# Kernel tuning notes

Hardware: AMD Instinct MI355X
Metric: run time of the kernel (lower is better)

Reference implementation:

```python
import jax, jax.numpy as jnp
import numpy as np

N, IN, HID, OUT, C, H = 50000, 1488, 1024, 512, 32, 8
E = 800000

def setup_inputs() -> dict:
    key = jax.random.key(0)
    ks = jax.random.split(key, 16)
    s = lambda k, shape, fan: jax.random.normal(k, shape, jnp.float32) * (1.0 / np.sqrt(fan))
    return {
        "x": jax.random.normal(ks[0], (N, IN), jnp.float32),
        "edge_index": jax.random.randint(ks[1], (2, E), 0, N, jnp.int64),
        "ln_g": jnp.ones((IN,), jnp.float32),
        "ln_b": jnp.zeros((IN,), jnp.float32),
        "W1": s(ks[2], (IN, HID), IN), "b1": jnp.zeros((HID,), jnp.float32),
        "W2": s(ks[3], (HID, OUT), HID), "b2": jnp.zeros((OUT,), jnp.float32),
        "Wr": s(ks[4], (OUT, C * H), OUT), "br": jnp.zeros((C * H,), jnp.float32),
        "Wg": s(ks[5], (OUT, C * H), OUT),
        "att_src": s(ks[6], (H, C), C),
        "att_dst": s(ks[7], (H, C), C),
        "bg": jnp.zeros((C * H,), jnp.float32),
    }

def reference(x, edge_index, ln_g, ln_b, W1, b1, W2, b2, Wr, br, Wg, att_src, att_dst, bg):
    n = x.shape[0]
    # LayerNorm
    mu = jnp.mean(x, axis=-1, keepdims=True)
    var = jnp.mean(jnp.square(x - mu), axis=-1, keepdims=True)
    xn = (x - mu) * jax.lax.rsqrt(var + 1e-5) * ln_g + ln_b
    # init_proj MLP
    h = jax.nn.relu(xn @ W1 + b1) @ W2 + b2            # [N, OUT]
    res = h @ Wr + br                                   # [N, H*C]
    # GATConv (add_self_loops=True, dropout inactive in eval)
    loops = jnp.arange(n, dtype=edge_index.dtype)
    src = jnp.concatenate([edge_index[0], loops])
    dst = jnp.concatenate([edge_index[1], loops])
    g = (h @ Wg).reshape(n, H, C)                       # [N, H, C]
    a_src = jnp.sum(g * att_src, axis=-1)               # [N, H]
    a_dst = jnp.sum(g * att_dst, axis=-1)               # [N, H]
    e = jax.nn.leaky_relu(a_src[src] + a_dst[dst], 0.2) # [E', H]
    m = jax.ops.segment_max(e, dst, num_segments=n)     # per-dst softmax (stable)
    ex = jnp.exp(e - m[dst])
    denom = jax.ops.segment_sum(ex, dst, num_segments=n)
    alpha = ex / (denom[dst] + 1e-16)                   # [E', H]
    msg = alpha[:, :, None] * g[src]                    # [E', H, C]
    agg = jax.ops.segment_sum(msg, dst, num_segments=n) # [N, H, C]
    out = agg.reshape(n, H * C) + bg
    return jax.nn.elu(out) + res
```

## Files before the change

### kernel.cpp

```cpp
#include <hip/hip_runtime.h>
#include <hip/hip_bf16.h>
#include <cstdint>
#include <cstddef>

#define NND 50000
#define DIN 1488
#define DINP 1536
#define DHID 1024
#define DOUT 512
#define DHC 256
#define NE 800000
#define NHD 8
#define SPLITC 256

typedef __attribute__((ext_vector_type(8))) short short8;
typedef __attribute__((ext_vector_type(4))) short short4v;
typedef __attribute__((ext_vector_type(4))) float f32x4;
typedef __attribute__((ext_vector_type(4))) int int4v;
typedef unsigned short ushort_t;

__device__ __forceinline__ unsigned short f2bf(float f){
  union { float f; unsigned u; } v; v.f = f;
  unsigned r = v.u + 0x7fffu + ((v.u >> 16) & 1u);
  return (unsigned short)(r >> 16);
}
__device__ __forceinline__ float bf2f(unsigned short u){
  union { unsigned u; float f; } v; v.u = ((unsigned)u) << 16;
  return v.f;
}

__device__ __forceinline__ void async16(const void* g, void* l){
  __builtin_amdgcn_global_load_lds((__attribute__((address_space(1))) void*)g,
                                   (__attribute__((address_space(3))) void*)l, 16, 0, 0);
}

__device__ __forceinline__ void tc_tile(const float* __restrict__ W,
                                        ushort_t* __restrict__ WT,
                                        int K, int Nn, int Kp, int bx, int by){
  __shared__ float tile[32][33];
  const int tx = threadIdx.x & 31, ty = threadIdx.x >> 5;
  const int k0 = bx*32, n0 = by*32;
  for (int i = ty; i < 32; i += 8){
    int k = k0 + i, n = n0 + tx;
    tile[i][tx] = (k < K && n < Nn) ? W[(size_t)k*Nn + n] : 0.f;
  }
  __syncthreads();
  for (int i = ty; i < 32; i += 8){
    int n = n0 + i, k = k0 + tx;
    if (n < Nn && k < Kp) WT[(size_t)n*Kp + k] = f2bf(tile[tx][i]);
  }
}

#define F1_CNT  3125
#define F1_LN   (F1_CNT + 12500)
__global__ __launch_bounds__(256) void fused1(const float* __restrict__ x,
                                              const float* __restrict__ gw,
                                              const float* __restrict__ bw,
                                              ushort_t* __restrict__ xn,
                                              const int* __restrict__ ei,
                                              int* __restrict__ cnt,
                                              const float* W1, const float* Wr,
                                              const float* Wg, const float* W2,
                                              const float* b2, const float* br,
                                              ushort_t* W1T, ushort_t* WrgT,
                                              ushort_t* W2bf, float* b2rg){
  const int bid = blockIdx.x;
  if (bid < F1_CNT){
    int e = bid*256 + threadIdx.x;
    if (e < NE) atomicAdd(&cnt[ei[NE + e]], 1);
    return;
  }
  if (bid < F1_LN){
    const int wid = threadIdx.x >> 6, lane = threadIdx.x & 63;
    const int row = (bid - F1_CNT)*4 + wid;
    if (row >= NND) return;
    const float* xr = x + (size_t)row * DIN;
    f32x4 xv[6];
    float s = 0.f, sq = 0.f;
    #pragma unroll
    for (int it = 0; it < 6; ++it){
      const int i = lane*4 + it*256;
      xv[it] = (i < DIN) ? *(const f32x4*)(xr + i) : (f32x4){0.f,0.f,0.f,0.f};
      s  += xv[it].x + xv[it].y + xv[it].z + xv[it].w;
      sq += xv[it].x*xv[it].x + xv[it].y*xv[it].y + xv[it].z*xv[it].z + xv[it].w*xv[it].w;
    }
    #pragma unroll
    for (int o = 32; o; o >>= 1){ s += __shfl_xor(s, o); sq += __shfl_xor(sq, o); }
    const float mu = s * (1.f/DIN);
    const float var = sq * (1.f/DIN) - mu*mu;
    const float rstd = rsqrtf(var + 1e-5f);
    ushort_t* xo = xn + (size_t)row * DINP;
    #pragma unroll
    for (int it = 0; it < 6; ++it){
      const int i = lane*4 + it*256;
      if (i < DIN){
        f32x4 gg = *(const f32x4*)(gw + i);
        f32x4 bb = *(const f32x4*)(bw + i);
        union { ushort_t u[4]; unsigned long long q; } o;
        o.u[0] = f2bf((xv[it].x-mu)*rstd*gg.x + bb.x);
        o.u[1] = f2bf((xv[it].y-mu)*rstd*gg.y + bb.y);
        o.u[2] = f2bf((xv[it].z-mu)*rstd*gg.z + bb.z);
        o.u[3] = f2bf((xv[it].w-mu)*rstd*gg.w + bb.w);
        *(unsigned long long*)(xo + i) = o.q;
      }
    }
    if (lane < (DINP - DIN)) xo[DIN + lane] = 0;
    return;
  }
  {
    int b = bid - F1_LN;
    if (b < 1536){ tc_tile(W1, W1T, DIN, DHID, DINP, b % 48, b / 48); return; }
    b -= 1536;
    if (b < 128){ tc_tile(Wr, WrgT, DOUT, DHC, DOUT, b % 16, b / 16); return; }
    b -= 128;
    if (b < 128){ tc_tile(Wg, WrgT + 256*DOUT, DOUT, DHC, DOUT, b % 16, b / 16); return; }
    b -= 128;
    if (b < 256){
      const int idx = (b*256 + threadIdx.x)*8;
      f32x4 v0 = *(const f32x4*)(W2 + idx);
      f32x4 v1 = *(const f32x4*)(W2 + idx + 4);
      union { ushort_t u[8]; short8 s; } o;
      o.u[0]=f2bf(v0.x); o.u[1]=f2bf(v0.y); o.u[2]=f2bf(v0.z); o.u[3]=f2bf(v0.w);
      o.u[4]=f2bf(v1.x); o.u[5]=f2bf(v1.y); o.u[6]=f2bf(v1.z); o.u[7]=f2bf(v1.w);
      *(short8*)(W2bf + idx) = o.s;
      return;
    }
    b -= 256;
    {
      const int c = b*256 + threadIdx.x;
      float acc = 0.f;
      if (c < 256){
        for (int j = 0; j < DOUT; ++j) acc += b2[j]*Wr[(size_t)j*DHC + c];
        acc += br[c];
      } else {
        const int cc = c - 256;
        for (int j = 0; j < DOUT; ++j) acc += b2[j]*Wg[(size_t)j*DHC + cc];
      }
      b2rg[c] = acc;
      return;
    }
  }
}

__device__ __forceinline__ void g256p8_body(ushort_t (&lds)[2][2][2][64*128],
                                            const ushort_t* __restrict__ A,
                                            const ushort_t* __restrict__ BT,
                                            const float* __restrict__ bias,
                                            ushort_t* __restrict__ out0,
                                            int M, int Nn, int K,
                                            int bid, int nwg, bool act){
  const int t = threadIdx.x, wid = t >> 6, lane = t & 63;
  const int CB = Nn >> 8;
  const int q = nwg >> 3, r = nwg & 7;
  const int xcd = bid & 7, slot = bid >> 3;
  const int lg = (xcd < r ? xcd*(q+1) : r*(q+1) + (xcd - r)*q) + slot;
  const int brow = (lg / CB) * 256, bcol = (lg % CB) * 256;

  const int l8  = t >> 3;
  const int cb  = (t & 7) << 4;
  const unsigned scb = (unsigned)(cb ^ ((l8 & 7) << 4));
  unsigned rowA[2][2], rowB[2][2];
  #pragma unroll
  for (int hf = 0; hf < 2; ++hf)
    #pragma unroll
    for (int rd = 0; rd < 2; ++rd){
      int ra = brow + hf*128 + rd*64 + l8; ra = ra < M ? ra : M-1;
      int rb = bcol + hf*128 + rd*64 + l8; rb = rb < Nn ? rb : Nn-1;
      rowA[hf][rd] = (unsigned)ra * (unsigned)(K*2);
      rowB[hf][rd] = (unsigned)rb * (unsigned)(K*2);
    }
  const int w8 = wid * 8;

#define STG_A(buf, hf, kt) do {                                               \
    const unsigned _ob = (unsigned)(kt)*128u + scb;                           \
    async16((const char*)A + rowA[hf][0] + _ob, &lds[buf][0][hf][(w8)*64]);   \
    async16((const char*)A + rowA[hf][1] + _ob, &lds[buf][0][hf][(64+w8)*64]);\
  } while(0)
#define STG_B(buf, hf, kt) do {                                               \
    const unsigned _ob = (unsigned)(kt)*128u + scb;                           \
    async16((const char*)BT + rowB[hf][0] + _ob, &lds[buf][1][hf][(w8)*64]);  \
    async16((const char*)BT + rowB[hf][1] + _ob, &lds[buf][1][hf][(64+w8)*64]);\
  } while(0)

  f32x4 acc[8][4];
  #pragma unroll
  for (int i=0;i<8;i++)
    #pragma unroll
    for (int j=0;j<4;j++) acc[i][j] = (f32x4){0.f,0.f,0.f,0.f};

  const int wrow = (wid >> 2), wcol = (wid & 3);
  const int fr = lane & 15;
  const int kb0 = (lane >> 4) << 4;
  const int sx  = (fr & 7) << 4;
  const int ko0 = ((kb0      ) ^ sx) >> 1;
  const int ko1 = ((kb0 | 64 ) ^ sx) >> 1;
  const int bhalf = wcol >> 1, brl = (wcol & 1)*64;

#define RD_A(buf, m) do {                                          \
    const int _ra = ((m)*16 + fr)*64;                              \
    af[m][0] = *(const short8*)&lds[buf][0][wrow][_ra + ko0];      \
    af[m][1] = *(const short8*)&lds[buf][0][wrow][_ra + ko1];      \
  } while(0)
#define RD_B(buf, n) do {                                          \
    const int _rb = (brl + (n)*16 + fr)*64;                        \
    bf[n][0] = *(const short8*)&lds[buf][1][bhalf][_rb + ko0];     \
    bf[n][1] = *(const short8*)&lds[buf][1][bhalf][_rb + ko1];     \
  } while(0)
#define SYNC_PH() do {                                             \
    __builtin_amdgcn_s_barrier();                                  \
    asm volatile("s_waitcnt lgkmcnt(0)" ::: "memory");             \
    __builtin_amdgcn_sched_barrier(0);                             \
  } while(0)
#define MFMA_Q(M0, N0) do {                                        \
    __builtin_amdgcn_s_setprio(1);                                 \
    _Pragma("unroll")                                              \
    for (int _m=(M0); _m<(M0)+4; ++_m)                             \
      _Pragma("unroll")                                            \
      for (int _n=(N0); _n<(N0)+2; ++_n){                          \
        acc[_m][_n] = __builtin_amdgcn_mfma_f32_16x16x32_bf16(af[_m][0], bf[_n][0], acc[_m][_n], 0, 0, 0); \
        acc[_m][_n] = __builtin_amdgcn_mfma_f32_16x16x32_bf16(af[_m][1], bf[_n][1], acc[_m][_n], 0, 0, 0); \
      }                                                            \
    __builtin_amdgcn_s_setprio(0);                                 \
  } while(0)

  const int nk = K >> 6;
  STG_A(0,0,0); STG_A(0,1,0); STG_B(0,0,0); STG_B(0,1,0);
  STG_A(1,0,1); STG_A(1,1,1);
  asm volatile("s_waitcnt vmcnt(4)" ::: "memory");
  __builtin_amdgcn_s_barrier();

  for (int kt = 0; kt < nk; ++kt){
    const int buf = kt & 1, obuf = buf ^ 1;
    short8 af[8][2], bf[4][2];
    RD_A(buf,0); RD_A(buf,1); RD_A(buf,2); RD_A(buf,3);
    RD_B(buf,0); RD_B(buf,1);
    if (kt + 1 < nk) STG_B(obuf, 0, kt + 1);
    SYNC_PH();
    MFMA_Q(0, 0);
    RD_A(buf,4); RD_A(buf,5); RD_A(buf,6); RD_A(buf,7);
    if (kt + 1 < nk) STG_B(obuf, 1, kt + 1);
    SYNC_PH();
    MFMA_Q(4, 0);
    RD_B(buf,2); RD_B(buf,3);
    if (kt + 2 < nk) STG_A(buf, 0, kt + 2);
    SYNC_PH();
    MFMA_Q(0, 2);
    if (kt + 2 < nk){
      STG_A(buf, 1, kt + 2);
      asm volatile("s_waitcnt vmcnt(4)" ::: "memory");
    } else {
      asm volatile("s_waitcnt vmcnt(0)" ::: "memory");
    }
    __builtin_amdgcn_s_barrier();
    MFMA_Q(4, 2);
  }
#undef STG_A
#undef STG_B
#undef RD_A
#undef RD_B
#undef SYNC_PH
#undef MFMA_Q

  float bv[4];
  #pragma unroll
  for (int n=0;n<4;n++){
    const int col = bcol + wcol*64 + n*16 + (lane & 15);
    bv[n] = bias ? bias[col] : 0.f;
  }
  ushort_t* sB = (ushort_t*)&lds[0][0][0][0];
  __syncthreads();
  #pragma unroll
  for (int m=0;m<8;m++){
    const int row = wrow*128 + m*16 + (lane >> 4)*4;
    #pragma unroll
    for (int n=0;n<4;n++){
      const int col = wcol*64 + n*16 + (lane & 15);
      #pragma unroll
      for (int j=0;j<4;j++){
        float v = acc[m][n][j] + bv[n];
        if (act) v = v > 0.f ? v : 0.f;
        sB[(row+j)*256 + col] = f2bf(v);
      }
    }
  }
  __syncthreads();
  const int srow = t >> 5, scol8 = (t & 31) * 8;
  #pragma unroll
  for (int rr = 0; rr < 16; ++rr){
    const int rloc = rr*16 + srow;
    const int grow = brow + rloc;
    if (grow < M)
      *(short8*)(out0 + (size_t)grow*Nn + bcol + scol8) = *(const short8*)&sB[rloc*256 + scol8];
  }
}

__global__ __launch_bounds__(512, 1) void mega_gemm(const ushort_t* __restrict__ xn,
                                                    const ushort_t* __restrict__ W1T,
                                                    const float* __restrict__ b1,
                                                    ushort_t* __restrict__ h1,
                                                    const ushort_t* __restrict__ WrgT,
                                                    const ushort_t* __restrict__ W2bf,
                                                    ushort_t* __restrict__ WcT,
                                                    const int* __restrict__ cnt,
                                                    int* __restrict__ offs,
                                                    int* __restrict__ cur){
  __shared__ __align__(16) ushort_t lds[2][2][2][64*128];
  const int t = threadIdx.x;

  if (blockIdx.x == 0){
    int* sbuf = (int*)&lds[0][0][0][0];
    const int chunk = (NND + 255) >> 8;
    int s = 0;
    if (t < 256){
      const int s0 = t*chunk;
      const int s1 = (s0 + chunk < NND) ? s0 + chunk : NND;
      for (int i = s0; i < s1; i += 4){
        int4v v = *(const int4v*)(cnt + i);
        s += v.x + v.y + v.z + v.w + 4;
      }
    }
    sbuf[t] = s; __syncthreads();
    for (int o = 1; o < 256; o <<= 1){
      int xv = (t >= o && t < 256) ? sbuf[t-o] : 0;
      __syncthreads();
      if (t < 256) sbuf[t] += xv;
      __syncthreads();
    }
    if (t < 256){
      int run = sbuf[t] - s;
      const int s0 = t*chunk;
      const int s1 = (s0 + chunk < NND) ? s0 + chunk : NND;
      for (int i = s0; i < s1; i += 4){
        int4v v = *(const int4v*)(cnt + i);
        int4v cu;
        cu.x = run; run += v.x + 1;
        cu.y = run; run += v.y + 1;
        cu.z = run; run += v.z + 1;
        cu.w = run; run += v.w + 1;
        *(int4v*)(cur + i)  = cu;
        *(int4v*)(offs + i) = cu;
      }
      if (t == 255) offs[NND] = run;
    }
    return;
  }
  if (blockIdx.x < 9){
    g256p8_body(lds, WrgT, W2bf, nullptr, WcT, 512, 1024, 512,
                (int)blockIdx.x - 1, 8, false);
    return;
  }
  g256p8_body(lds, xn, W1T, b1, h1, NND, DHID, DINP,
              (int)blockIdx.x - 9, (int)gridDim.x - 9, true);
}

#define G2_NWG 392
template<int ACT, int MODE, int CB, int EXTRA>
__global__ __launch_bounds__(512, 2) void gemm256(const ushort_t* __restrict__ A,
                                                  const ushort_t* __restrict__ BT,
                                                  const float* __restrict__ bias,
                                                  void* __restrict__ out0,
                                                  void* __restrict__ out1,
                                                  int M, int Nn, int K,
                                                  const int* __restrict__ ei,
                                                  int* __restrict__ cur,
                                                  int* __restrict__ eidx,
                                                  const float* __restrict__ att_s,
                                                  const float* __restrict__ att_d,
                                                  float* __restrict__ asrc,
                                                  float* __restrict__ adst){
  __shared__ __align__(16) ushort_t lds[2][2][256*64];
  const int t = threadIdx.x, wid = t >> 6, lane = t & 63;

  if (EXTRA == 1 && blockIdx.x >= G2_NWG){
    int i = (blockIdx.x - G2_NWG)*512 + t;
    if (i < NND){
      int p = atomicAdd(&cur[i], 1); eidx[p] = i;
    } else if (i < NND + NE){
      int e = i - NND;
      int src = ei[e], dst = ei[NE + e];
      int p = atomicAdd(&cur[dst], 1);
      eidx[p] = src;
    }
    return;
  }

  const int bid = blockIdx.x, nwg = G2_NWG;
  const int q = nwg >> 3, r = nwg & 7;
  const int xcd = bid & 7, slot = bid >> 3;
  const int lg = (xcd < r ? xcd*(q+1) : r*(q+1) + (xcd - r)*q) + slot;
  const int brow = (lg / CB) * 256, bcol = (lg % CB) * 256;

  const int l8  = t >> 3;
  const int cb  = (t & 7) << 4;
  const unsigned scb = (unsigned)(cb ^ ((l8 & 7) << 4));
  unsigned rowA[4], rowB[4];
  #pragma unroll
  for (int rd = 0; rd < 4; ++rd){
    int ra = brow + rd*64 + l8; ra = ra < M ? ra : M-1;
    int rb = bcol + rd*64 + l8; rb = rb < Nn ? rb : Nn-1;
    rowA[rd] = (unsigned)ra * (unsigned)(K*2);
    rowB[rd] = (unsigned)rb * (unsigned)(K*2);
  }
  const int wst = (wid * 8) * 64;

#define STAGE2(buf, kt) do {                                              \
    const unsigned _ob = (unsigned)(kt)*128u + scb;                       \
    _Pragma("unroll")                                                     \
    for (int _rd = 0; _rd < 4; ++_rd){                                    \
      async16((const char*)A  + rowA[_rd] + _ob, &lds[buf][0][_rd*64*64 + wst]); \
      async16((const char*)BT + rowB[_rd] + _ob, &lds[buf][1][_rd*64*64 + wst]); \
    }                                                                     \
  } while(0)

  f32x4 acc[8][4];
  #pragma unroll
  for (int i=0;i<8;i++)
    #pragma unroll
    for (int j=0;j<4;j++) acc[i][j] = (f32x4){0.f,0.f,0.f,0.f};

  const int wrow = (wid >> 2), wcol = (wid & 3);
  const int fr = lane & 15;
  const int kb0 = (lane >> 4) << 4;
  const int sx  = (fr & 7) << 4;
  const int ko0 = ((kb0      ) ^ sx) >> 1;
  const int ko1 = ((kb0 | 64 ) ^ sx) >> 1;

  const int nk = K >> 6;
  STAGE2(0, 0);
  STAGE2(1, 1);
  for (int kt = 0; kt < nk; ++kt){
    const ushort_t* bA = lds[kt & 1][0];
    const ushort_t* bB = lds[kt & 1][1];
    if (kt + 1 < nk) asm volatile("s_waitcnt vmcnt(8)" ::: "memory");
    else             asm volatile("s_waitcnt vmcnt(0)" ::: "memory");
    __builtin_amdgcn_s_barrier();
    short8 af[8][2], bf_[4][2];
    #pragma unroll
    for (int m=0;m<8;m++){
      const int ra = (wrow*128 + m*16 + fr)*64;
      af[m][0] = *(const short8*)&bA[ra + ko0];
      af[m][1] = *(const short8*)&bA[ra + ko1];
    }
    #pragma unroll
    for (int n=0;n<4;n++){
      const int rb = (wcol*64 + n*16 + fr)*64;
      bf_[n][0] = *(const short8*)&bB[rb + ko0];
      bf_[n][1] = *(const short8*)&bB[rb + ko1];
    }
    asm volatile("s_waitcnt lgkmcnt(0)" ::: "memory");
    __builtin_amdgcn_sched_barrier(0);
    __builtin_amdgcn_s_barrier();
    if (kt + 2 < nk) STAGE2(kt & 1, kt + 2);
    __builtin_amdgcn_s_setprio(1);
    #pragma unroll
    for (int m=0;m<8;m++)
      #pragma unroll
      for (int n=0;n<4;n++){
        acc[m][n] = __builtin_amdgcn_mfma_f32_16x16x32_bf16(af[m][0], bf_[n][0], acc[m][n], 0, 0, 0);
        acc[m][n] = __builtin_amdgcn_mfma_f32_16x16x32_bf16(af[m][1], bf_[n][1], acc[m][n], 0, 0, 0);
      }
    __builtin_amdgcn_s_setprio(0);
  }
#undef STAGE2

  const bool isf32 = (MODE == 0) || (MODE == 2 && bcol == 0);
  float bv[4];
  #pragma unroll
  for (int n=0;n<4;n++){
    const int col = bcol + wcol*64 + n*16 + (lane & 15);
    float b = 0.f;
    if (MODE == 1){ if (bias) b = bias[col]; }
    if (MODE == 2){ b = bias[col]; }
    bv[n] = b;
  }

  if (isf32){
    float* outF; int ostride, ocb;
    if (MODE == 0){ outF = (float*)out0; ostride = Nn;  ocb = bcol; }
    else          { outF = (float*)out0; ostride = 256; ocb = 0;    }
    float* sF = (float*)&lds[0][0][0];
    #pragma unroll
    for (int p = 0; p < 2; ++p){
      __syncthreads();
      if (wrow == p){
        #pragma unroll
        for (int m=0;m<8;m++){
          const int row = m*16 + (lane >> 4)*4;
          #pragma unroll
          for (int n=0;n<4;n++){
            const int col = wcol*64 + n*16 + (lane & 15);
            #pragma unroll
            for (int j=0;j<4;j++){
              float v = acc[m][n][j] + bv[n];
              if (ACT) v = v > 0.f ? v : 0.f;
              sF[(row+j)*256 + col] = v;
            }
          }
        }
      }
      __syncthreads();
      const int srow = t >> 6, scol4 = (t & 63) * 4;
      #pragma unroll
      for (int rr = 0; rr < 16; ++rr){
        const int rloc = rr*8 + srow;
        const int grow = brow + p*128 + rloc;
        if (grow < M)
          *(f32x4*)(outF + (size_t)grow*ostride + ocb + scol4) = *(const f32x4*)&sF[rloc*256 + scol4];
      }
    }
  } else {
    ushort_t* outB; int ostride, ocb;
    if (MODE == 1){ outB = (ushort_t*)out0; ostride = Nn;  ocb = bcol; }
    else          { outB = (ushort_t*)out1; ostride = 256; ocb = 0;    }
    ushort_t* sB = (ushort_t*)&lds[0][0][0];
    __syncthreads();
    #pragma unroll
    for (int m=0;m<8;m++){
      const int row = wrow*128 + m*16 + (lane >> 4)*4;
      #pragma unroll
      for (int n=0;n<4;n++){
        const int col = wcol*64 + n*16 + (lane & 15);
        #pragma unroll
        for (int j=0;j<4;j++){
          float v = acc[m][n][j] + bv[n];
          if (ACT) v = v > 0.f ? v : 0.f;
          sB[(row+j)*256 + col] = f2bf(v);
        }
      }
    }
    __syncthreads();
    const int srow = t >> 5, scol8 = (t & 31) * 8;
    #pragma unroll
    for (int rr = 0; rr < 16; ++rr){
      const int rloc = rr*16 + srow;
      const int grow = brow + rloc;
      if (grow < M)
        *(short8*)(outB + (size_t)grow*ostride + ocb + scol8) = *(const short8*)&sB[rloc*256 + scol8];
    }
    if (MODE == 2){
      const int h = t & 7;
      const int hc0 = h * 32;
      #pragma unroll
      for (int k = 0; k < 4; ++k){
        const int rloc = (t >> 3) + k*64;
        const int grow = brow + rloc;
        if (grow < M){
          float a = 0.f, d = 0.f;
          #pragma unroll
          for (int c0 = 0; c0 < 32; c0 += 8){
            short8 gv = *(const short8*)&sB[rloc*256 + hc0 + c0];
            #pragma unroll
            for (int j = 0; j < 8; ++j){
              float g = bf2f((ushort_t)gv[j]);
              a += g*att_s[hc0 + c0 + j];
              d += g*att_d[hc0 + c0 + j];
            }
          }
          asrc[grow*NHD + h] = a;
          adst[grow*NHD + h] = d;
        }
      }
    }
  }
}

__global__ __launch_bounds__(256) void gat_agg(const int* __restrict__ offs,
                                               const int* __restrict__ eidx,
                                               const float* __restrict__ asrc,
                                               const float* __restrict__ adst,
                                               const ushort_t* __restrict__ gm,
                                               const float* __restrict__ res,
                                               const float* __restrict__ bg,
                                               float* __restrict__ out){
  const int wid = threadIdx.x >> 6, lane = threadIdx.x & 63;
  const int node = blockIdx.x*4 + wid;
  if (node >= NND) return;
  const int h = lane >> 3, jj = lane & 7;
  const int e0 = offs[node], deg = offs[node+1] - e0;
  const float adv = adst[node*NHD + h];

  float mx = -1e30f;
  for (int j = jj; j < deg; j += 8){
    int s = eidx[e0 + j];
    float e = asrc[s*NHD + h] + adv; e = e > 0.f ? e : 0.2f*e;
    mx = fmaxf(mx, e);
  }
  mx = fmaxf(mx, __shfl_xor(mx, 1));
  mx = fmaxf(mx, __shfl_xor(mx, 2));
  mx = fmaxf(mx, __shfl_xor(mx, 4));

  const int c4 = lane*4;
  float sm = 0.f;
  f32x4 acc = {0.f,0.f,0.f,0.f};
  for (int j0 = 0; j0 < deg; j0 += 8){
    const int cnt = (deg - j0) < 8 ? (deg - j0) : 8;
    int s = 0; float w = 0.f;
    if (jj < cnt){
      s = eidx[e0 + j0 + jj];
      float e = asrc[s*NHD + h] + adv; e = e > 0.f ? e : 0.2f*e;
      w = __expf(e - mx);
      sm += w;
    }
    #pragma unroll
    for (int u = 0; u < 8; ++u){
      if (u < cnt){
        const int   su = __builtin_amdgcn_readlane(s, u);
        const float wu = __shfl(w, (h << 3) | u);
        short4v gv = *(const short4v*)(gm + (size_t)su*DHC + c4);
        acc.x += wu*bf2f((ushort_t)gv.x);
        acc.y += wu*bf2f((ushort_t)gv.y);
        acc.z += wu*bf2f((ushort_t)gv.z);
        acc.w += wu*bf2f((ushort_t)gv.w);
      }
    }
  }
  sm += __shfl_xor(sm, 1); sm += __shfl_xor(sm, 2); sm += __shfl_xor(sm, 4);
  const float inv = 1.f/(sm + 1e-16f);

  f32x4 bgv = *(const f32x4*)(bg + c4);
  f32x4 rv  = *(const f32x4*)(res + (size_t)node*DHC + c4);
  f32x4 o;
  #pragma unroll
  for (int q = 0; q < 4; ++q){
    float v = acc[q]*inv + bgv[q];
    v = v > 0.f ? v : expm1f(v);
    o[q] = v + rv[q];
  }
  *(f32x4*)(out + (size_t)node*DHC + c4) = o;
}

extern "C" void kernel_launch(void* const* d_in, const int* in_sizes, int n_in,
                              void* d_out, int out_size, void* d_ws, size_t ws_size,
                              hipStream_t stream){
  (void)in_sizes; (void)n_in; (void)out_size; (void)ws_size;
  const float* x     = (const float*)d_in[0];
  const int*   ei    = (const int*)d_in[1];
  const float* ln_g  = (const float*)d_in[2];
  const float* ln_b  = (const float*)d_in[3];
  const float* W1    = (const float*)d_in[4];
  const float* b1    = (const float*)d_in[5];
  const float* W2    = (const float*)d_in[6];
  const float* b2    = (const float*)d_in[7];
  const float* Wr    = (const float*)d_in[8];
  const float* br    = (const float*)d_in[9];
  const float* Wg    = (const float*)d_in[10];
  const float* att_s = (const float*)d_in[11];
  const float* att_d = (const float*)d_in[12];
  const float* bg    = (const float*)d_in[13];
  float* out = (float*)d_out;

  char* p = (char*)d_ws;
  ushort_t* xn   = (ushort_t*)(p);
  ushort_t* h1   = (ushort_t*)(p + 153600000);
  float*    asrc = (float*)(p + 256000000);
  float*    adst = (float*)(p + 257600000);
  int*      cnt  = (int*)(p + 259200000);
  int*      offs = (int*)(p + 259400064);
  int*      cur  = (int*)(p + 259600128);
  int*      eidx = (int*)(p + 259800192);
  ushort_t* W1T  = (ushort_t*)d_out;
  ushort_t* WrgT = (ushort_t*)((char*)d_out + 3145728);
  ushort_t* W2bf = (ushort_t*)((char*)d_out + 3670016);
  ushort_t* WcT  = (ushort_t*)((char*)d_out + 4718592);
  float*    b2rg = (float*)((char*)d_out + 5767168);
  float*    res  = (float*)(p + 0);
  ushort_t* gm   = (ushort_t*)(p + 51200000);

  hipMemsetAsync(cnt, 0, NND*sizeof(int), stream);

  fused1<<<F1_LN + 2050, 256, 0, stream>>>(
      x, ln_g, ln_b, xn, ei, cnt,
      W1, Wr, Wg, W2, b2, br, W1T, WrgT, W2bf, b2rg);

  mega_gemm<<<793, 512, 0, stream>>>(xn, W1T, b1, h1, WrgT, W2bf, WcT,
                                     cnt, offs, cur);

  gemm256<0,2,2,1><<<G2_NWG + (NND + NE + 511)/512, 512, 0, stream>>>(
      h1, WcT, b2rg, res, gm, NND, 2*DHC, DHID,
      ei, cur, eidx, att_s, att_d, asrc, adst);

  gat_agg<<<(NND + 3)/4, 256, 0, stream>>>(offs, eidx, asrc, adst, gm, res, bg, out);
}
```

Before: 489.6 us.

## Port third GEMM to 8-phase interleaved pipeline and widen LayerNorm stores

The third GEMM (h1 × [Wr|Wg]) becomes a specialized kernel that reuses the mega_gemm 8-phase schedule. That schedule interleaves LDS fragment reads, global prefetch of split A/B halves and MFMA quarters, replacing the simpler two-stage loop where all reads finished before any compute. The aim is to hide load latency behind MFMA, at the cost of occupancy dropping to one workgroup per CU via launch bounds. Separately, LayerNorm now handles 8 elements per lane and writes 16-byte stores, including the zero padding, in place of 8-byte stores plus a separate pad write.

```diff
diff --git a/kernel.cpp b/kernel.cpp
--- a/kernel.cpp
+++ b/kernel.cpp
@@ -11,7 +11,6 @@
 #define DHC 256
 #define NE 800000
 #define NHD 8
-#define SPLITC 256
 
 typedef __attribute__((ext_vector_type(8))) short short8;
 typedef __attribute__((ext_vector_type(4))) short short4v;
@@ -75,14 +74,22 @@
     const int row = (bid - F1_CNT)*4 + wid;
     if (row >= NND) return;
     const float* xr = x + (size_t)row * DIN;
-    f32x4 xv[6];
+    f32x4 xa[3], xb[3];
     float s = 0.f, sq = 0.f;
     #pragma unroll
-    for (int it = 0; it < 6; ++it){
-      const int i = lane*4 + it*256;
-      xv[it] = (i < DIN) ? *(const f32x4*)(xr + i) : (f32x4){0.f,0.f,0.f,0.f};
-      s  += xv[it].x + xv[it].y + xv[it].z + xv[it].w;
-      sq += xv[it].x*xv[it].x + xv[it].y*xv[it].y + xv[it].z*xv[it].z + xv[it].w*xv[it].w;
+    for (int it = 0; it < 3; ++it){
+      const int i = lane*8 + it*512;
+      if (i < DIN){
+        xa[it] = *(const f32x4*)(xr + i);
+        xb[it] = *(const f32x4*)(xr + i + 4);
+      } else {
+        xa[it] = (f32x4){0.f,0.f,0.f,0.f};
+        xb[it] = (f32x4){0.f,0.f,0.f,0.f};
+      }
+      s  += xa[it].x + xa[it].y + xa[it].z + xa[it].w
+          + xb[it].x + xb[it].y + xb[it].z + xb[it].w;
+      sq += xa[it].x*xa[it].x + xa[it].y*xa[it].y + xa[it].z*xa[it].z + xa[it].w*xa[it].w
+          + xb[it].x*xb[it].x + xb[it].y*xb[it].y + xb[it].z*xb[it].z + xb[it].w*xb[it].w;
     }
     #pragma unroll
     for (int o = 32; o; o >>= 1){ s += __shfl_xor(s, o); sq += __shfl_xor(sq, o); }
@@ -91,20 +98,27 @@
     const float rstd = rsqrtf(var + 1e-5f);
     ushort_t* xo = xn + (size_t)row * DINP;
     #pragma unroll
-    for (int it = 0; it < 6; ++it){
-      const int i = lane*4 + it*256;
+    for (int it = 0; it < 3; ++it){
+      const int i = lane*8 + it*512;
+      union { ushort_t u[8]; short8 v; } o;
       if (i < DIN){
-        f32x4 gg = *(const f32x4*)(gw + i);
-        f32x4 bb = *(const f32x4*)(bw + i);
-        union { ushort_t u[4]; unsigned long long q; } o;
-        o.u[0] = f2bf((xv[it].x-mu)*rstd*gg.x + bb.x);
-        o.u[1] = f2bf((xv[it].y-mu)*rstd*gg.y + bb.y);
-        o.u[2] = f2bf((xv[it].z-mu)*rstd*gg.z + bb.z);
-        o.u[3] = f2bf((xv[it].w-mu)*rstd*gg.w + bb.w);
-        *(unsigned long long*)(xo + i) = o.q;
-      }
-    }
-    if (lane < (DINP - DIN)) xo[DIN + lane] = 0;
+        f32x4 ga = *(const f32x4*)(gw + i);
+        f32x4 gb = *(const f32x4*)(gw + i + 4);
+        f32x4 ba = *(const f32x4*)(bw + i);
+        f32x4 bb = *(const f32x4*)(bw + i + 4);
+        o.u[0] = f2bf((xa[it].x-mu)*rstd*ga.x + ba.x);
+        o.u[1] = f2bf((xa[it].y-mu)*rstd*ga.y + ba.y);
+        o.u[2] = f2bf((xa[it].z-mu)*rstd*ga.z + ba.z);
+        o.u[3] = f2bf((xa[it].w-mu)*rstd*ga.w + ba.w);
+        o.u[4] = f2bf((xb[it].x-mu)*rstd*gb.x + bb.x);
+        o.u[5] = f2bf((xb[it].y-mu)*rstd*gb.y + bb.y);
+        o.u[6] = f2bf((xb[it].z-mu)*rstd*gb.z + bb.z);
+        o.u[7] = f2bf((xb[it].w-mu)*rstd*gb.w + bb.w);
+      } else {
+        o.u[0]=o.u[1]=o.u[2]=o.u[3]=o.u[4]=o.u[5]=o.u[6]=o.u[7]=0;
+      }
+      *(short8*)(xo + i) = o.v;
+    }
     return;
   }
   {
@@ -254,12 +268,6 @@
     __builtin_amdgcn_s_barrier();
     MFMA_Q(4, 2);
   }
-#undef STG_A
-#undef STG_B
-#undef RD_A
-#undef RD_B
-#undef SYNC_PH
-#undef MFMA_Q
 
   float bv[4];
   #pragma unroll
@@ -353,14 +361,12 @@
               (int)blockIdx.x - 9, (int)gridDim.x - 9, true);
 }
 
-#define G2_NWG 392
-template<int ACT, int MODE, int CB, int EXTRA>
-__global__ __launch_bounds__(512, 2) void gemm256(const ushort_t* __restrict__ A,
+#define G3_NWG 392
+__global__ __launch_bounds__(512, 1) void gemm3p8(const ushort_t* __restrict__ A,
                                                   const ushort_t* __restrict__ BT,
                                                   const float* __restrict__ bias,
-                                                  void* __restrict__ out0,
-                                                  void* __restrict__ out1,
-                                                  int M, int Nn, int K,
+                                                  float* __restrict__ res,
+                                                  ushort_t* __restrict__ gm,
                                                   const int* __restrict__ ei,
                                                   int* __restrict__ cur,
                                                   int* __restrict__ eidx,
@@ -368,11 +374,11 @@
                                                   const float* __restrict__ att_d,
                                                   float* __restrict__ asrc,
                                                   float* __restrict__ adst){
-  __shared__ __align__(16) ushort_t lds[2][2][256*64];
+  __shared__ __align__(16) ushort_t lds[2][2][2][64*128];
   const int t = threadIdx.x, wid = t >> 6, lane = t & 63;
 
-  if (EXTRA == 1 && blockIdx.x >= G2_NWG){
-    int i = (blockIdx.x - G2_NWG)*512 + t;
+  if (blockIdx.x >= G3_NWG){
+    int i = (blockIdx.x - G3_NWG)*512 + t;
     if (i < NND){
       int p = atomicAdd(&cur[i], 1); eidx[p] = i;
     } else if (i < NND + NE){
@@ -384,7 +390,9 @@
     return;
   }
 
-  const int bid = blockIdx.x, nwg = G2_NWG;
+  const int M = NND, Nn = 512, K = DHID;
+  const int bid = blockIdx.x, nwg = G3_NWG;
+  const int CB = 2;
   const int q = nwg >> 3, r = nwg & 7;
   const int xcd = bid & 7, slot = bid >> 3;
   const int lg = (xcd < r ? xcd*(q+1) : r*(q+1) + (xcd - r)*q) + slot;
@@ -393,24 +401,17 @@
   const int l8  = t >> 3;
   const int cb  = (t & 7) << 4;
   const unsigned scb = (unsigned)(cb ^ ((l8 & 7) << 4));
-  unsigned rowA[4], rowB[4];
-  #pragma unroll
-  for (int rd = 0; rd < 4; ++rd){
-    int ra = brow + rd*64 + l8; ra = ra < M ? ra : M-1;
-    int rb = bcol + rd*64 + l8; rb = rb < Nn ? rb : Nn-1;
-    rowA[rd] = (unsigned)ra * (unsigned)(K*2);
-    rowB[rd] = (unsigned)rb * (unsigned)(K*2);
-  }
-  const int wst = (wid * 8) * 64;
-
-#define STAGE2(buf, kt) do {                                              \
-    const unsigned _ob = (unsigned)(kt)*128u + scb;                       \
-    _Pragma("unroll")                                                     \
-    for (int _rd = 0; _rd < 4; ++_rd){                                    \
-      async16((const char*)A  + rowA[_rd] + _ob, &lds[buf][0][_rd*64*64 + wst]); \
-      async16((const char*)BT + rowB[_rd] + _ob, &lds[buf][1][_rd*64*64 + wst]); \
-    }                                                                     \
-  } while(0)
+  unsigned rowA[2][2], rowB[2][2];
+  #pragma unroll
+  for (int hf = 0; hf < 2; ++hf)
+    #pragma unroll
+    for (int rd = 0; rd < 2; ++rd){
+      int ra = brow + hf*128 + rd*64 + l8; ra = ra < M ? ra : M-1;
+      int rb = bcol + hf*128 + rd*64 + l8; rb = rb < Nn ? rb : Nn-1;
+      rowA[hf][rd] = (unsigned)ra * (unsigned)(K*2);
+      rowB[hf][rd] = (unsigned)rb * (unsigned)(K*2);
+    }
+  const int w8 = wid * 8;
 
   f32x4 acc[8][4];
   #pragma unroll
@@ -424,61 +425,54 @@
   const int sx  = (fr & 7) << 4;
   const int ko0 = ((kb0      ) ^ sx) >> 1;
   const int ko1 = ((kb0 | 64 ) ^ sx) >> 1;
+  const int bhalf = wcol >> 1, brl = (wcol & 1)*64;
 
   const int nk = K >> 6;
-  STAGE2(0, 0);
-  STAGE2(1, 1);
+  STG_A(0,0,0); STG_A(0,1,0); STG_B(0,0,0); STG_B(0,1,0);
+  STG_A(1,0,1); STG_A(1,1,1);
+  asm volatile("s_waitcnt vmcnt(4)" ::: "memory");
+  __builtin_amdgcn_s_barrier();
+
   for (int kt = 0; kt < nk; ++kt){
-    const ushort_t* bA = lds[kt & 1][0];
-    const ushort_t* bB = lds[kt & 1][1];
-    if (kt + 1 < nk) asm volatile("s_waitcnt vmcnt(8)" ::: "memory");
-    else             asm volatile("s_waitcnt vmcnt(0)" ::: "memory");
+    const int buf = kt & 1, obuf = buf ^ 1;
+    short8 af[8][2], bf[4][2];
+    RD_A(buf,0); RD_A(buf,1); RD_A(buf,2); RD_A(buf,3);
+    RD_B(buf,0); RD_B(buf,1);
+    if (kt + 1 < nk) STG_B(obuf, 0, kt + 1);
+    SYNC_PH();
+    MFMA_Q(0, 0);
+    RD_A(buf,4); RD_A(buf,5); RD_A(buf,6); RD_A(buf,7);
+    if (kt + 1 < nk) STG_B(obuf, 1, kt + 1);
+    SYNC_PH();
+    MFMA_Q(4, 0);
+    RD_B(buf,2); RD_B(buf,3);
+    if (kt + 2 < nk) STG_A(buf, 0, kt + 2);
+    SYNC_PH();
+    MFMA_Q(0, 2);
+    if (kt + 2 < nk){
+      STG_A(buf, 1, kt + 2);
+      asm volatile("s_waitcnt vmcnt(4)" ::: "memory");
+    } else {
+      asm volatile("s_waitcnt vmcnt(0)" ::: "memory");
+    }
     __builtin_amdgcn_s_barrier();
-    short8 af[8][2], bf_[4][2];
-    #pragma unroll
-    for (int m=0;m<8;m++){
-      const int ra = (wrow*128 + m*16 + fr)*64;
-      af[m][0] = *(const short8*)&bA[ra + ko0];
-      af[m][1] = *(const short8*)&bA[ra + ko1];
-    }
-    #pragma unroll
-    for (int n=0;n<4;n++){
-      const int rb = (wcol*64 + n*16 + fr)*64;
-      bf_[n][0] = *(const short8*)&bB[rb + ko0];
-      bf_[n][1] = *(const short8*)&bB[rb + ko1];
-    }
-    asm volatile("s_waitcnt lgkmcnt(0)" ::: "memory");
-    __builtin_amdgcn_sched_barrier(0);
-    __builtin_amdgcn_s_barrier();
-    if (kt + 2 < nk) STAGE2(kt & 1, kt + 2);
-    __builtin_amdgcn_s_setprio(1);
-    #pragma unroll
-    for (int m=0;m<8;m++)
-      #pragma unroll
-      for (int n=0;n<4;n++){
-        acc[m][n] = __builtin_amdgcn_mfma_f32_16x16x32_bf16(af[m][0], bf_[n][0], acc[m][n], 0, 0, 0);
-        acc[m][n] = __builtin_amdgcn_mfma_f32_16x16x32_bf16(af[m][1], bf_[n][1], acc[m][n], 0, 0, 0);
-      }
-    __builtin_amdgcn_s_setprio(0);
-  }
-#undef STAGE2
-
-  const bool isf32 = (MODE == 0) || (MODE == 2 && bcol == 0);
+    MFMA_Q(4, 2);
+  }
+#undef STG_A
+#undef STG_B
+#undef RD_A
+#undef RD_B
+#undef SYNC_PH
+#undef MFMA_Q
+
   float bv[4];
   #pragma unroll
   for (int n=0;n<4;n++){
     const int col = bcol + wcol*64 + n*16 + (lane & 15);
-    float b = 0.f;
-    if (MODE == 1){ if (bias) b = bias[col]; }
-    if (MODE == 2){ b = bias[col]; }
-    bv[n] = b;
-  }
-
-  if (isf32){
-    float* outF; int ostride, ocb;
-    if (MODE == 0){ outF = (float*)out0; ostride = Nn;  ocb = bcol; }
-    else          { outF = (float*)out0; ostride = 256; ocb = 0;    }
-    float* sF = (float*)&lds[0][0][0];
+    bv[n] = bias[col];
+  }
+  if (bcol == 0){
+    float* sF = (float*)&lds[0][0][0][0];
     #pragma unroll
     for (int p = 0; p < 2; ++p){
       __syncthreads();
@@ -490,11 +484,8 @@
           for (int n=0;n<4;n++){
             const int col = wcol*64 + n*16 + (lane & 15);
             #pragma unroll
-            for (int j=0;j<4;j++){
-              float v = acc[m][n][j] + bv[n];
-              if (ACT) v = v > 0.f ? v : 0.f;
-              sF[(row+j)*256 + col] = v;
-            }
+            for (int j=0;j<4;j++)
+              sF[(row+j)*256 + col] = acc[m][n][j] + bv[n];
           }
         }
       }
@@ -505,14 +496,11 @@
         const int rloc = rr*8 + srow;
         const int grow = brow + p*128 + rloc;
         if (grow < M)
-          *(f32x4*)(outF + (size_t)grow*ostride + ocb + scol4) = *(const f32x4*)&sF[rloc*256 + scol4];
+          *(f32x4*)(res + (size_t)grow*256 + scol4) = *(const f32x4*)&sF[rloc*256 + scol4];
       }
     }
   } else {
-    ushort_t* outB; int ostride, ocb;
-    if (MODE == 1){ outB = (ushort_t*)out0; ostride = Nn;  ocb = bcol; }
-    else          { outB = (ushort_t*)out1; ostride = 256; ocb = 0;    }
-    ushort_t* sB = (ushort_t*)&lds[0][0][0];
+    ushort_t* sB = (ushort_t*)&lds[0][0][0][0];
     __syncthreads();
     #pragma unroll
     for (int m=0;m<8;m++){
@@ -521,11 +509,8 @@
       for (int n=0;n<4;n++){
         const int col = wcol*64 + n*16 + (lane & 15);
         #pragma unroll
-        for (int j=0;j<4;j++){
-          float v = acc[m][n][j] + bv[n];
-          if (ACT) v = v > 0.f ? v : 0.f;
-          sB[(row+j)*256 + col] = f2bf(v);
-        }
+        for (int j=0;j<4;j++)
+          sB[(row+j)*256 + col] = f2bf(acc[m][n][j] + bv[n]);
       }
     }
     __syncthreads();
@@ -535,30 +520,28 @@
       const int rloc = rr*16 + srow;
       const int grow = brow + rloc;
       if (grow < M)
-        *(short8*)(outB + (size_t)grow*ostride + ocb + scol8) = *(const short8*)&sB[rloc*256 + scol8];
-    }
-    if (MODE == 2){
-      const int h = t & 7;
-      const int hc0 = h * 32;
-      #pragma unroll
-      for (int k = 0; k < 4; ++k){
-        const int rloc = (t >> 3) + k*64;
-        const int grow = brow + rloc;
-        if (grow < M){
-          float a = 0.f, d = 0.f;
+        *(short8*)(gm + (size_t)grow*256 + scol8) = *(const short8*)&sB[rloc*256 + scol8];
+    }
+    const int h = t & 7;
+    const int hc0 = h * 32;
+    #pragma unroll
+    for (int k = 0; k < 4; ++k){
+      const int rloc = (t >> 3) + k*64;
+      const int grow = brow + rloc;
+      if (grow < M){
+        float a = 0.f, d = 0.f;
+        #pragma unroll
+        for (int c0 = 0; c0 < 32; c0 += 8){
+          short8 gv = *(const short8*)&sB[rloc*256 + hc0 + c0];
           #pragma unroll
-          for (int c0 = 0; c0 < 32; c0 += 8){
-            short8 gv = *(const short8*)&sB[rloc*256 + hc0 + c0];
-            #pragma unroll
-            for (int j = 0; j < 8; ++j){
-              float g = bf2f((ushort_t)gv[j]);
-              a += g*att_s[hc0 + c0 + j];
-              d += g*att_d[hc0 + c0 + j];
-            }
+          for (int j = 0; j < 8; ++j){
+            float g = bf2f((ushort_t)gv[j]);
+            a += g*att_s[hc0 + c0 + j];
+            d += g*att_d[hc0 + c0 + j];
           }
-          asrc[grow*NHD + h] = a;
-          adst[grow*NHD + h] = d;
         }
+        asrc[grow*NHD + h] = a;
+        adst[grow*NHD + h] = d;
       }
     }
   }
@@ -675,8 +658,8 @@
   mega_gemm<<<793, 512, 0, stream>>>(xn, W1T, b1, h1, WrgT, W2bf, WcT,
                                      cnt, offs, cur);
 
-  gemm256<0,2,2,1><<<G2_NWG + (NND + NE + 511)/512, 512, 0, stream>>>(
-      h1, WcT, b2rg, res, gm, NND, 2*DHC, DHID,
+  gemm3p8<<<G3_NWG + (NND + NE + 511)/512, 512, 0, stream>>>(
+      h1, WcT, b2rg, res, gm,
       ei, cur, eidx, att_s, att_d, asrc, adst);
 
   gat_agg<<<(NND + 3)/4, 256, 0, stream>>>(offs, eidx, asrc, adst, gm, res, bg, out);
```

Result: no change. 481.8 us (-1.6%).
